# Kernel tuning notes

Hardware: AMD Instinct MI355X
Metric: run time of the kernel (lower is better)

The kernel has to match this reference:

```python
import jax, jax.numpy as jnp
import numpy as np

N_POINTS = 8192
D_FEAT = 256
WEIGHT = 1.0  # self.weight
EPS = 1e-12


def _pairwise_dist(x):
    # Euclidean pairwise distances, [N, N]
    sq = jnp.sum(x * x, axis=-1)
    d2 = sq[:, None] + sq[None, :] - 2.0 * (x @ x.T)
    d2 = jnp.maximum(d2, 0.0)
    return jnp.sqrt(d2 + EPS)


def _mst_edge_weights(dist):
    # Prim's algorithm, vectorized O(N^2). The MST edge lengths are exactly
    # the death times of the H0 (dim-0) persistence diagram of the
    # Vietoris-Rips filtration (all births = 0). jit-compatible via lax.scan.
    n = dist.shape[0]
    big = jnp.asarray(1e30, dist.dtype)
    in_tree0 = jnp.zeros((n,), dtype=bool).at[0].set(True)
    mindist0 = dist[0]

    def step(carry, _):
        in_tree, mindist = carry
        masked = jnp.where(in_tree, big, mindist)
        j = jnp.argmin(masked)
        w = masked[j]                      # weight of MST edge added this step
        in_tree = in_tree.at[j].set(True)
        mindist = jnp.minimum(mindist, dist[j])
        return (in_tree, mindist), w

    _, weights = jax.lax.scan(step, (in_tree0, mindist0), None, length=n - 1)
    return weights  # [N-1] H0 death times


def _persistent_entropy(lifetimes):
    # PersistentEntropy.compute: p_i = l_i / sum(l); E = -sum p_i log p_i
    total = jnp.sum(lifetimes)
    p = lifetimes / (total + EPS)
    return -jnp.sum(p * jnp.log(p + EPS))


def setup_inputs() -> dict:
    key = jax.random.key(0)
    representations = jax.random.normal(key, (N_POINTS, D_FEAT), dtype=jnp.float32)
    return {"representations": representations}


def reference(representations):
    # PersistentHomology.compute_from_distance: VR filtration over the point
    # cloud; H0 diagram computed exactly via MST (single-linkage). Higher
    # dims (dim=1) are not produced, so the `if dim < len(diagrams)` guard
    # skips them, matching GPU PH implementations that emit H0 only.
    dist = _pairwise_dist(representations)
    deaths = _mst_edge_weights(dist)
    entropy = _persistent_entropy(deaths)
    loss = -entropy  # target_entropy is None -> maximize entropy
    return WEIGHT * loss
```

## Files before the change

### kernel.cpp

```cpp
#include <hip/hip_runtime.h>
#include <hip/hip_bf16.h>
#include <hip/hip_fp16.h>

#define NP 8192
#define DF 256
#define NROUNDS 13

typedef unsigned long long u64;
typedef unsigned short u16;
using bf16x8 = __attribute__((ext_vector_type(8))) short;
using f32x4  = __attribute__((ext_vector_type(4))) float;
using u16x8  = __attribute__((ext_vector_type(8))) u16;

__device__ __forceinline__ u16 f2bf(float f) {
  __hip_bfloat16 h = __float2bfloat16(f);
  return __builtin_bit_cast(u16, h);
}


__global__ void init_kernel(int* comp, u64* compmin, int* edgeCnt, int* nComps) {
  int i = blockIdx.x * 256 + threadIdx.x;
  if (i < NP) { comp[i] = i; compmin[i] = ~0ull; }
  if (i == 0) { *edgeCnt = 0; *nComps = NP; }
}


__global__ __launch_bounds__(64) void sq_kernel(const float* __restrict__ X, float* __restrict__ sq) {
  int i = blockIdx.x;
  float4 v = ((const float4*)(X + (size_t)i * DF))[threadIdx.x];
  float s = v.x * v.x + v.y * v.y + v.z * v.z + v.w * v.w;
#pragma unroll
  for (int off = 32; off >= 1; off >>= 1) s += __shfl_down(s, off);
  if (threadIdx.x == 0) sq[i] = s;
}


__global__ __launch_bounds__(256) void cvt_kernel(const float* __restrict__ X, u16* __restrict__ Xb) {
  int idx = (blockIdx.x * 256 + threadIdx.x) * 8;
  float4 a = ((const float4*)(X + idx))[0];
  float4 b = ((const float4*)(X + idx))[1];
  u16x8 o;
  o[0] = f2bf(a.x); o[1] = f2bf(a.y); o[2] = f2bf(a.z); o[3] = f2bf(a.w);
  o[4] = f2bf(b.x); o[5] = f2bf(b.y); o[6] = f2bf(b.z); o[7] = f2bf(b.w);
  *(u16x8*)(Xb + idx) = o;
}


template <bool PRE>
__global__ __launch_bounds__(256) void build_dist_kernel(
    const float* __restrict__ X, const u16* __restrict__ Xb,
    const float* __restrict__ sq, _Float16* __restrict__ d2) {
  __shared__ __align__(16) u16 At[128 * 40];
  __shared__ __align__(16) u16 Bt[128 * 40];
  const int t = threadIdx.x;
  const int m0 = blockIdx.y * 128, n0 = blockIdx.x * 128;
  const int wid = t >> 6, lane = t & 63;
  const int wm = wid >> 1, wn = wid & 1;
  const int lrow = lane & 15, lk = lane >> 4;
  f32x4 acc[4][4] = {};

  const int srow = t >> 1, shalf = t & 1;
  for (int k0 = 0; k0 < DF; k0 += 32) {
    u16x8 av0, av1, bv0, bv1;
    if (PRE) {
      const u16* pa = Xb + (size_t)(m0 + srow) * DF + k0 + shalf * 16;
      av0 = *(const u16x8*)pa; av1 = *(const u16x8*)(pa + 8);
      const u16* pb = Xb + (size_t)(n0 + srow) * DF + k0 + shalf * 16;
      bv0 = *(const u16x8*)pb; bv1 = *(const u16x8*)(pb + 8);
    } else {
      const float4* pa = (const float4*)(X + (size_t)(m0 + srow) * DF + k0 + shalf * 16);
      float4 a0 = pa[0], a1 = pa[1], a2 = pa[2], a3 = pa[3];
      av0[0]=f2bf(a0.x); av0[1]=f2bf(a0.y); av0[2]=f2bf(a0.z); av0[3]=f2bf(a0.w);
      av0[4]=f2bf(a1.x); av0[5]=f2bf(a1.y); av0[6]=f2bf(a1.z); av0[7]=f2bf(a1.w);
      av1[0]=f2bf(a2.x); av1[1]=f2bf(a2.y); av1[2]=f2bf(a2.z); av1[3]=f2bf(a2.w);
      av1[4]=f2bf(a3.x); av1[5]=f2bf(a3.y); av1[6]=f2bf(a3.z); av1[7]=f2bf(a3.w);
      const float4* pb = (const float4*)(X + (size_t)(n0 + srow) * DF + k0 + shalf * 16);
      float4 b0 = pb[0], b1 = pb[1], b2 = pb[2], b3 = pb[3];
      bv0[0]=f2bf(b0.x); bv0[1]=f2bf(b0.y); bv0[2]=f2bf(b0.z); bv0[3]=f2bf(b0.w);
      bv0[4]=f2bf(b1.x); bv0[5]=f2bf(b1.y); bv0[6]=f2bf(b1.z); bv0[7]=f2bf(b1.w);
      bv1[0]=f2bf(b2.x); bv1[1]=f2bf(b2.y); bv1[2]=f2bf(b2.z); bv1[3]=f2bf(b2.w);
      bv1[4]=f2bf(b3.x); bv1[5]=f2bf(b3.y); bv1[6]=f2bf(b3.z); bv1[7]=f2bf(b3.w);
    }
    __syncthreads();
    *(u16x8*)&At[srow * 40 + shalf * 16] = av0;
    *(u16x8*)&At[srow * 40 + shalf * 16 + 8] = av1;
    *(u16x8*)&Bt[srow * 40 + shalf * 16] = bv0;
    *(u16x8*)&Bt[srow * 40 + shalf * 16 + 8] = bv1;
    __syncthreads();
    bf16x8 af[4], bfr[4];
#pragma unroll
    for (int fm = 0; fm < 4; ++fm)
      af[fm] = *(const bf16x8*)&At[(wm * 64 + fm * 16 + lrow) * 40 + lk * 8];
#pragma unroll
    for (int fn = 0; fn < 4; ++fn)
      bfr[fn] = *(const bf16x8*)&Bt[(wn * 64 + fn * 16 + lrow) * 40 + lk * 8];
#pragma unroll
    for (int fm = 0; fm < 4; ++fm)
#pragma unroll
      for (int fn = 0; fn < 4; ++fn)
        acc[fm][fn] = __builtin_amdgcn_mfma_f32_16x16x32_bf16(af[fm], bfr[fn], acc[fm][fn], 0, 0, 0);
  }

  float sqj[4];
#pragma unroll
  for (int fn = 0; fn < 4; ++fn) sqj[fn] = sq[n0 + wn * 64 + fn * 16 + lrow];
#pragma unroll
  for (int fm = 0; fm < 4; ++fm) {
#pragma unroll
    for (int r = 0; r < 4; ++r) {
      int i = m0 + wm * 64 + fm * 16 + lk * 4 + r;
      float si = sq[i];
#pragma unroll
      for (int fn = 0; fn < 4; ++fn) {
        int j = n0 + wn * 64 + fn * 16 + lrow;
        float dd = si + sqj[fn] - 2.0f * acc[fm][fn][r];
        dd = fmaxf(dd, 0.0f);
        if (i == j) dd = INFINITY;
        d2[(size_t)i * NP + j] = (_Float16)dd;
      }
    }
  }
}


__global__ __launch_bounds__(256) void row_min_kernel(
    const _Float16* __restrict__ d2, const int* __restrict__ comp,
    u64* __restrict__ compmin, const int* __restrict__ nComps) {
  if (*nComps == 1) return;
  const int i = blockIdx.x;
  const int ci = comp[i];
  const u16* row = (const u16*)(d2 + (size_t)i * NP);
  u64 best = ~0ull;
  for (int base = threadIdx.x * 8; base < NP; base += 256 * 8) {
    u16x8 v = *(const u16x8*)(row + base);
    int4 c0 = *(const int4*)(comp + base);
    int4 c1 = *(const int4*)(comp + base + 4);
    int cs[8] = {c0.x, c0.y, c0.z, c0.w, c1.x, c1.y, c1.z, c1.w};
#pragma unroll
    for (int q = 0; q < 8; ++q) {
      if (cs[q] != ci) {
        int j = base + q;
        int lo = i < j ? i : j;
        int hi = i ^ j ^ lo;
        u64 k = ((u64)v[q] << 26) | ((u64)lo << 13) | (u64)hi;
        best = k < best ? k : best;
      }
    }
  }
#pragma unroll
  for (int off = 32; off >= 1; off >>= 1) {
    u64 o = __shfl_down(best, off);
    best = best < o ? best : o;
  }
  __shared__ u64 sred[4];
  const int lane = threadIdx.x & 63, wv = threadIdx.x >> 6;
  if (lane == 0) sred[wv] = best;
  __syncthreads();
  if (threadIdx.x == 0) {
    best = sred[0];
#pragma unroll
    for (int w = 1; w < 4; ++w) best = best < sred[w] ? best : sred[w];
    if (best != ~0ull) atomicMin(&compmin[ci], best);
  }
}


__global__ void select_kernel(const float* __restrict__ X, const float* __restrict__ sq,
                              const int* __restrict__ comp, const u64* __restrict__ compmin,
                              int* __restrict__ parent, float* __restrict__ edgeW,
                              int* __restrict__ edgeCnt, const int* __restrict__ nComps) {
  int c = blockIdx.x * blockDim.x + threadIdx.x;
  if (c >= NP) return;
  if (*nComps == 1) { parent[c] = c; return; }
  u64 m = compmin[c];
  if (m == ~0ull) { parent[c] = c; return; }
  int a = (int)((m >> 13) & 0x1FFF);
  int b = (int)(m & 0x1FFF);
  int j = (comp[a] == c) ? b : a;
  int d = comp[j];
  bool mutual = false;
  u64 md = compmin[d];
  if (md != ~0ull) {
    int a2 = (int)((md >> 13) & 0x1FFF);
    int b2 = (int)(md & 0x1FFF);
    int j2 = (comp[a2] == d) ? b2 : a2;
    mutual = (comp[j2] == c);
  }
  if (mutual && c > d) { parent[c] = d; return; }
  parent[c] = mutual ? c : d;
  const float4* pa = (const float4*)(X + (size_t)a * DF);
  const float4* pb = (const float4*)(X + (size_t)b * DF);
  float dot = 0.f;
#pragma unroll 8
  for (int k = 0; k < DF / 4; ++k) {
    float4 va = pa[k], vb = pb[k];
    dot += va.x * vb.x + va.y * vb.y + va.z * vb.z + va.w * vb.w;
  }
  float dd = sq[a] + sq[b] - 2.f * dot;
  float w = sqrtf(fmaxf(dd, 0.f) + 1e-12f);
  int idx = atomicAdd(edgeCnt, 1);
  if (idx < NP) edgeW[idx] = w;
}


__global__ __launch_bounds__(1024) void jump_relabel_kernel(
    const int* __restrict__ parent, int* __restrict__ comp,
    u64* __restrict__ compmin, int* __restrict__ nComps) {
  if (*nComps == 1) return;
  __shared__ int sp[NP];
  __shared__ unsigned char fl[NP];
  __shared__ int scnt;
  const int t = threadIdx.x;
  for (int c = t; c < NP; c += 1024) { sp[c] = parent[c]; fl[c] = 0; }
  if (t == 0) scnt = 0;
  __syncthreads();
  for (int it = 0; it < 13; ++it) {
    for (int c = t; c < NP; c += 1024) sp[c] = sp[sp[c]];
    __syncthreads();
  }
  int part = 0;
  for (int i = t; i < NP; i += 1024) {
    int nc = sp[comp[i]];
    comp[i] = nc;
    fl[nc] = 1;
  }
  __syncthreads();
  for (int c = t; c < NP; c += 1024) part += fl[c];
#pragma unroll
  for (int off = 32; off >= 1; off >>= 1) part += __shfl_down(part, off);
  if ((t & 63) == 0) atomicAdd(&scnt, part);
  for (int c = t; c < NP; c += 1024) compmin[c] = ~0ull;
  __syncthreads();
  if (t == 0) *nComps = scnt;
}


__global__ __launch_bounds__(1024) void entropy_kernel(const float* __restrict__ edgeW,
                                                       const int* __restrict__ edgeCnt,
                                                       float* __restrict__ out) {
  __shared__ float sred[16];
  __shared__ float stot;
  int ne = *edgeCnt;
  if (ne > NP) ne = NP;
  float s = 0.f;
  for (int k = threadIdx.x; k < ne; k += 1024) s += edgeW[k];
#pragma unroll
  for (int off = 32; off >= 1; off >>= 1) s += __shfl_down(s, off);
  int lane = threadIdx.x & 63, wv = threadIdx.x >> 6;
  if (lane == 0) sred[wv] = s;
  __syncthreads();
  if (threadIdx.x == 0) {
    float tt = 0.f;
#pragma unroll
    for (int w = 0; w < 16; ++w) tt += sred[w];
    stot = tt;
  }
  __syncthreads();
  float total = stot;
  float acc = 0.f;
  for (int k = threadIdx.x; k < ne; k += 1024) {
    float p = edgeW[k] / (total + 1e-12f);
    acc += p * logf(p + 1e-12f);
  }
#pragma unroll
  for (int off = 32; off >= 1; off >>= 1) acc += __shfl_down(acc, off);
  if (lane == 0) sred[wv] = acc;
  __syncthreads();
  if (threadIdx.x == 0) {
    float tt = 0.f;
#pragma unroll
    for (int w = 0; w < 16; ++w) tt += sred[w];
    out[0] = tt;
  }
}


extern "C" void kernel_launch(void* const* d_in, const int* in_sizes, int n_in,
                              void* d_out, int out_size, void* d_ws, size_t ws_size,
                              hipStream_t stream) {
  const float* X = (const float*)d_in[0];
  float* out = (float*)d_out;
  char* ws = (char*)d_ws;

  const size_t nn = (size_t)NP * NP;
  size_t off = (nn * 2 + 255) & ~(size_t)255;
  _Float16* d2 = (_Float16*)ws;
  float* sq = (float*)(ws + off);      off += (size_t)NP * 4;
  int* comp = (int*)(ws + off);        off += (size_t)NP * 4;
  u64* compmin = (u64*)(ws + off);     off += (size_t)NP * 8;
  int* parent = (int*)(ws + off);      off += (size_t)NP * 4;
  float* edgeW = (float*)(ws + off);   off += (size_t)NP * 4;
  int* edgeCnt = (int*)(ws + off);     off += 64;
  int* nComps = (int*)(ws + off);      off += 64;
  off = (off + 255) & ~(size_t)255;
  u16* Xb = (u16*)(ws + off);
  const bool PRE = (ws_size >= off + (size_t)NP * DF * 2);

  init_kernel<<<NP / 256, 256, 0, stream>>>(comp, compmin, edgeCnt, nComps);
  sq_kernel<<<NP, 64, 0, stream>>>(X, sq);
  if (PRE) {
    cvt_kernel<<<NP * DF / (256 * 8), 256, 0, stream>>>(X, Xb);
    build_dist_kernel<true><<<dim3(NP / 128, NP / 128), 256, 0, stream>>>(X, Xb, sq, d2);
  } else {
    build_dist_kernel<false><<<dim3(NP / 128, NP / 128), 256, 0, stream>>>(X, Xb, sq, d2);
  }
  for (int r = 0; r < NROUNDS; ++r) {
    row_min_kernel<<<NP, 256, 0, stream>>>(d2, comp, compmin, nComps);
    select_kernel<<<NP / 256, 256, 0, stream>>>(X, sq, comp, compmin, parent, edgeW, edgeCnt, nComps);
    jump_relabel_kernel<<<1, 1024, 0, stream>>>(parent, comp, compmin, nComps);
  }
  entropy_kernel<<<1, 1024, 0, stream>>>(edgeW, edgeCnt, out);
}
```

Before: 395.3 us.

## Precompute per-row top-K candidate edges for Boruvka rounds with full-row fallback

Adds a one-time histogram-based pass that stores up to 48 nearest neighbours per row in a transposed candidate table. Each Boruvka round then scans only these candidates per thread instead of rereading the full 8192-wide fp16 row, and falls back to a full-row scan when no out-of-component candidate remains. The distance epilogue is also staged through shared memory so global stores are coalesced, and pointer jumping now exits early once it converges. The risks are the extra top-K pass, candT aliasing the Xb buffer (safe only because Xb is dead by then), and slow serial fallbacks once components grow large.

```diff
diff --git a/kernel.cpp b/kernel.cpp
--- a/kernel.cpp
+++ b/kernel.cpp
@@ -5,8 +5,11 @@
 #define NP 8192
 #define DF 256
 #define NROUNDS 13
+#define CAND_K 48
+#define NBINS 2048
 
 typedef unsigned long long u64;
+typedef unsigned int u32;
 typedef unsigned short u16;
 using bf16x8 = __attribute__((ext_vector_type(8))) short;
 using f32x4  = __attribute__((ext_vector_type(4))) float;
@@ -14,6 +17,10 @@
 
 __device__ __forceinline__ u16 f2bf(float f) {
   __hip_bfloat16 h = __float2bfloat16(f);
+  return __builtin_bit_cast(u16, h);
+}
+__device__ __forceinline__ u16 f2h_bits(float f) {
+  _Float16 h = (_Float16)f;
   return __builtin_bit_cast(u16, h);
 }
 
@@ -50,8 +57,9 @@
 __global__ __launch_bounds__(256) void build_dist_kernel(
     const float* __restrict__ X, const u16* __restrict__ Xb,
     const float* __restrict__ sq, _Float16* __restrict__ d2) {
-  __shared__ __align__(16) u16 At[128 * 40];
-  __shared__ __align__(16) u16 Bt[128 * 40];
+  __shared__ __align__(16) u16 smem[128 * 144];
+  u16* At = smem;
+  u16* Bt = smem + 128 * 40;
   const int t = threadIdx.x;
   const int m0 = blockIdx.y * 128, n0 = blockIdx.x * 128;
   const int wid = t >> 6, lane = t & 63;
@@ -100,6 +108,7 @@
       for (int fn = 0; fn < 4; ++fn)
         acc[fm][fn] = __builtin_amdgcn_mfma_f32_16x16x32_bf16(af[fm], bfr[fn], acc[fm][fn], 0, 0, 0);
   }
+  __syncthreads();
 
   float sqj[4];
 #pragma unroll
@@ -108,59 +117,175 @@
   for (int fm = 0; fm < 4; ++fm) {
 #pragma unroll
     for (int r = 0; r < 4; ++r) {
-      int i = m0 + wm * 64 + fm * 16 + lk * 4 + r;
+      int row = wm * 64 + fm * 16 + lk * 4 + r;
+      int i = m0 + row;
       float si = sq[i];
 #pragma unroll
       for (int fn = 0; fn < 4; ++fn) {
-        int j = n0 + wn * 64 + fn * 16 + lrow;
+        int col = wn * 64 + fn * 16 + lrow;
         float dd = si + sqj[fn] - 2.0f * acc[fm][fn][r];
         dd = fmaxf(dd, 0.0f);
-        if (i == j) dd = INFINITY;
-        d2[(size_t)i * NP + j] = (_Float16)dd;
+        if (i == n0 + col) dd = INFINITY;
+        smem[row * 144 + col] = f2h_bits(dd);
       }
     }
   }
-}
-
-
-__global__ __launch_bounds__(256) void row_min_kernel(
-    const _Float16* __restrict__ d2, const int* __restrict__ comp,
+  __syncthreads();
+#pragma unroll
+  for (int k = 0; k < 8; ++k) {
+    int flat = k * 256 + t;
+    int row = flat >> 4, cb = (flat & 15) * 8;
+    *(u16x8*)&d2[(size_t)(m0 + row) * NP + n0 + cb] = *(const u16x8*)&smem[row * 144 + cb];
+  }
+}
+
+
+__global__ __launch_bounds__(256) void topk_kernel(const _Float16* __restrict__ d2,
+                                                   u64* __restrict__ candT,
+                                                   u32* __restrict__ candCnt) {
+  __shared__ u16 rowbuf[NP];
+  __shared__ u32 hist[NBINS];
+  __shared__ u32 scanw[4];
+  __shared__ int swred[4];
+  __shared__ int sB;
+  __shared__ u32 sCnt;
+  const int i = blockIdx.x;
+  const int t = threadIdx.x;
+  const u16* row = (const u16*)(d2 + (size_t)i * NP);
+  for (int b = t; b < NBINS; b += 256) hist[b] = 0;
+  if (t == 0) sCnt = 0;
+  __syncthreads();
+  for (int base = t * 8; base < NP; base += 2048) {
+    u16x8 v = *(const u16x8*)(row + base);
+    *(u16x8*)&rowbuf[base] = v;
+#pragma unroll
+    for (int q = 0; q < 8; ++q) atomicAdd(&hist[v[q] >> 5], 1u);
+  }
+  __syncthreads();
+  u32 loc[8]; u32 s = 0;
+#pragma unroll
+  for (int q = 0; q < 8; ++q) { loc[q] = hist[t * 8 + q]; s += loc[q]; }
+  u32 pre = s;
+  for (int off = 1; off < 64; off <<= 1) {
+    u32 o = __shfl_up(pre, off);
+    if ((t & 63) >= off) pre += o;
+  }
+  if ((t & 63) == 63) scanw[t >> 6] = pre;
+  __syncthreads();
+  u32 wbase = 0;
+  for (int w = 0; w < (t >> 6); ++w) wbase += scanw[w];
+  u32 c = wbase + pre - s;
+  int lb = -1;
+#pragma unroll
+  for (int q = 0; q < 8; ++q) {
+    c += loc[q];
+    if (c >= 1 && c <= CAND_K) lb = t * 8 + q;
+  }
+#pragma unroll
+  for (int off = 32; off >= 1; off >>= 1) {
+    int o = __shfl_down(lb, off);
+    lb = lb > o ? lb : o;
+  }
+  if ((t & 63) == 0) swred[t >> 6] = lb;
+  __syncthreads();
+  if (t == 0) {
+    int m = swred[0];
+#pragma unroll
+    for (int w = 1; w < 4; ++w) m = m > swred[w] ? m : swred[w];
+    sB = m;
+  }
+  __syncthreads();
+  const int B = sB;
+  if (B >= 0) {
+    for (int base = t * 8; base < NP; base += 2048) {
+#pragma unroll
+      for (int q = 0; q < 8; ++q) {
+        u16 v = rowbuf[base + q];
+        if ((int)(v >> 5) <= B) {
+          u32 pos = atomicAdd(&sCnt, 1u);
+          if (pos < CAND_K) {
+            int j = base + q;
+            int lo = i < j ? i : j;
+            int hi = i ^ j ^ lo;
+            candT[(size_t)pos * NP + i] = ((u64)v << 26) | ((u64)lo << 13) | (u64)hi;
+          }
+        }
+      }
+    }
+  }
+  __syncthreads();
+  if (t == 0) {
+    u32 n = sCnt;
+    candCnt[i] = (n == 0 || n > CAND_K) ? 0x80000000u : n;
+  }
+}
+
+
+__global__ __launch_bounds__(256) void round_min_kernel(
+    const _Float16* __restrict__ d2, const u64* __restrict__ candT,
+    const u32* __restrict__ candCnt, const int* __restrict__ comp,
     u64* __restrict__ compmin, const int* __restrict__ nComps) {
   if (*nComps == 1) return;
-  const int i = blockIdx.x;
+  __shared__ int fbl[256];
+  __shared__ int fbn;
+  __shared__ u64 sred[4];
+  const int t = threadIdx.x;
+  const int i = blockIdx.x * 256 + t;
+  if (t == 0) fbn = 0;
+  __syncthreads();
   const int ci = comp[i];
-  const u16* row = (const u16*)(d2 + (size_t)i * NP);
+  u32 cc = candCnt[i];
+  int n = (int)(cc & 0x7fffffffu);
   u64 best = ~0ull;
-  for (int base = threadIdx.x * 8; base < NP; base += 256 * 8) {
-    u16x8 v = *(const u16x8*)(row + base);
-    int4 c0 = *(const int4*)(comp + base);
-    int4 c1 = *(const int4*)(comp + base + 4);
-    int cs[8] = {c0.x, c0.y, c0.z, c0.w, c1.x, c1.y, c1.z, c1.w};
-#pragma unroll
-    for (int q = 0; q < 8; ++q) {
-      if (cs[q] != ci) {
-        int j = base + q;
-        int lo = i < j ? i : j;
-        int hi = i ^ j ^ lo;
-        u64 k = ((u64)v[q] << 26) | ((u64)lo << 13) | (u64)hi;
-        best = k < best ? k : best;
+  for (int k = 0; k < n; ++k) {
+    u64 key = candT[(size_t)k * NP + i];
+    int lo = (int)((key >> 13) & 0x1FFF);
+    int hi = (int)(key & 0x1FFF);
+    int j = (lo == i) ? hi : lo;
+    if (comp[j] != ci && key < best) best = key;
+  }
+  if (best != ~0ull && !(cc & 0x80000000u)) {
+    atomicMin(&compmin[ci], best);
+  } else {
+    int p = atomicAdd(&fbn, 1);
+    fbl[p] = i;
+  }
+  __syncthreads();
+  for (int f = 0; f < fbn; ++f) {
+    int r = fbl[f];
+    int cr = comp[r];
+    const u16* rowp = (const u16*)(d2 + (size_t)r * NP);
+    u64 b2 = ~0ull;
+    for (int base = t * 8; base < NP; base += 2048) {
+      u16x8 v = *(const u16x8*)(rowp + base);
+      int4 c0 = *(const int4*)(comp + base);
+      int4 c1 = *(const int4*)(comp + base + 4);
+      int cs[8] = {c0.x, c0.y, c0.z, c0.w, c1.x, c1.y, c1.z, c1.w};
+#pragma unroll
+      for (int q = 0; q < 8; ++q) {
+        if (cs[q] != cr) {
+          int j = base + q;
+          int lo = r < j ? r : j;
+          int hi = r ^ j ^ lo;
+          u64 k = ((u64)v[q] << 26) | ((u64)lo << 13) | (u64)hi;
+          b2 = k < b2 ? k : b2;
+        }
       }
     }
-  }
-#pragma unroll
-  for (int off = 32; off >= 1; off >>= 1) {
-    u64 o = __shfl_down(best, off);
-    best = best < o ? best : o;
-  }
-  __shared__ u64 sred[4];
-  const int lane = threadIdx.x & 63, wv = threadIdx.x >> 6;
-  if (lane == 0) sred[wv] = best;
-  __syncthreads();
-  if (threadIdx.x == 0) {
-    best = sred[0];
-#pragma unroll
-    for (int w = 1; w < 4; ++w) best = best < sred[w] ? best : sred[w];
-    if (best != ~0ull) atomicMin(&compmin[ci], best);
+#pragma unroll
+    for (int off = 32; off >= 1; off >>= 1) {
+      u64 o = __shfl_down(b2, off);
+      b2 = b2 < o ? b2 : o;
+    }
+    if ((t & 63) == 0) sred[t >> 6] = b2;
+    __syncthreads();
+    if (t == 0) {
+      b2 = sred[0];
+#pragma unroll
+      for (int w = 1; w < 4; ++w) b2 = b2 < sred[w] ? b2 : sred[w];
+      if (b2 != ~0ull) atomicMin(&compmin[cr], b2);
+    }
+    __syncthreads();
   }
 }
 
@@ -210,12 +335,23 @@
   __shared__ int sp[NP];
   __shared__ unsigned char fl[NP];
   __shared__ int scnt;
+  __shared__ int sch;
   const int t = threadIdx.x;
   for (int c = t; c < NP; c += 1024) { sp[c] = parent[c]; fl[c] = 0; }
-  if (t == 0) scnt = 0;
-  __syncthreads();
-  for (int it = 0; it < 13; ++it) {
-    for (int c = t; c < NP; c += 1024) sp[c] = sp[sp[c]];
+  if (t == 0) { scnt = 0; sch = 0; }
+  __syncthreads();
+  for (int it = 0; it < NROUNDS; ++it) {
+    int ch = 0;
+    for (int c = t; c < NP; c += 1024) {
+      int p = sp[c];
+      int pp = sp[p];
+      if (p != pp) { sp[c] = pp; ch = 1; }
+    }
+    if (ch) sch = 1;
+    __syncthreads();
+    if (!sch) break;
+    __syncthreads();
+    if (t == 0) sch = 0;
     __syncthreads();
   }
   int part = 0;
@@ -290,10 +426,12 @@
   u64* compmin = (u64*)(ws + off);     off += (size_t)NP * 8;
   int* parent = (int*)(ws + off);      off += (size_t)NP * 4;
   float* edgeW = (float*)(ws + off);   off += (size_t)NP * 4;
+  u32* candCnt = (u32*)(ws + off);     off += (size_t)NP * 4;
   int* edgeCnt = (int*)(ws + off);     off += 64;
   int* nComps = (int*)(ws + off);      off += 64;
   off = (off + 255) & ~(size_t)255;
   u16* Xb = (u16*)(ws + off);
+  u64* candT = (u64*)(ws + off);
   const bool PRE = (ws_size >= off + (size_t)NP * DF * 2);
 
   init_kernel<<<NP / 256, 256, 0, stream>>>(comp, compmin, edgeCnt, nComps);
@@ -304,8 +442,9 @@
   } else {
     build_dist_kernel<false><<<dim3(NP / 128, NP / 128), 256, 0, stream>>>(X, Xb, sq, d2);
   }
+  topk_kernel<<<NP, 256, 0, stream>>>(d2, candT, candCnt);
   for (int r = 0; r < NROUNDS; ++r) {
-    row_min_kernel<<<NP, 256, 0, stream>>>(d2, comp, compmin, nComps);
+    round_min_kernel<<<NP / 256, 256, 0, stream>>>(d2, candT, candCnt, comp, compmin, nComps);
     select_kernel<<<NP / 256, 256, 0, stream>>>(X, sq, comp, compmin, parent, edgeW, edgeCnt, nComps);
     jump_relabel_kernel<<<1, 1024, 0, stream>>>(parent, comp, compmin, nComps);
   }
```

Result: slower. 428.4 us (+8.4%).
